# Kernel tuning notes

Measured on AMD Instinct MI355X. Metric: run time of the kernel, lower is better.

The kernel has to match this reference:

```python
import jax, jax.numpy as jnp
import numpy as np

N = 100000        # nodes
DEG = 16          # fixed neighbor count per node
E = N * DEG       # total edges
D = 128           # node feature dim
DE = 16           # edge feature dim
DOUT = 128


def setup_inputs() -> dict:
    key = jax.random.key(0)
    k1, k2, k3, k4, k5 = jax.random.split(key, 5)
    h = jax.random.normal(k1, (N, D), dtype=jnp.float32)
    edge_table = jax.random.normal(k2, (E, DE), dtype=jnp.float32)
    # xavier-uniform-ish init for W (2D + DE, DOUT)
    fan_in, fan_out = 2 * D + DE, DOUT
    limit = float(np.sqrt(6.0 / (fan_in + fan_out)))
    W = jax.random.uniform(k3, (fan_in, fan_out), dtype=jnp.float32,
                           minval=-limit, maxval=limit)
    neighbor_idx = jax.random.randint(k4, (E,), 0, N, dtype=jnp.int64)
    edge_idx = jax.random.randint(k5, (E,), 0, E, dtype=jnp.int64)
    segment_ids = jnp.repeat(jnp.arange(N, dtype=jnp.int64), DEG)  # sorted, fixed degree
    return {"h": h, "edge_table": edge_table, "W": W,
            "neighbor_idx": neighbor_idx, "edge_idx": edge_idx,
            "segment_ids": segment_ids}


def reference(h, edge_table, W, neighbor_idx, edge_idx, segment_ids):
    # ragged gather: per-edge neighbor node feats + edge feats -> [E, D+DE]
    nf = jnp.take(h, neighbor_idx, axis=0)                 # [E, D]
    ef = jnp.take(edge_table, edge_idx, axis=0)            # [E, DE]
    cat = jnp.concatenate([nf, ef], axis=1)                # [E, D+DE]
    # per-node segment mean (ragged reduce)
    sums = jax.ops.segment_sum(cat, segment_ids, num_segments=N)          # [N, D+DE]
    counts = jax.ops.segment_sum(jnp.ones((cat.shape[0], 1), cat.dtype),
                                 segment_ids, num_segments=N)             # [N, 1]
    mean = sums / jnp.maximum(counts, 1.0)
    feat = jnp.concatenate([h, mean], axis=1)              # [N, 2D+DE]
    return jax.nn.elu(feat @ W)                            # [N, DOUT]
```

## Files before the change

kernel.cpp:

```cpp
#include <hip/hip_runtime.h>
#include <cstdint>

#define NNODES 100000
#define NDEG 16
#define DFEAT 128
#define DEDGE 16
#define KDIM  272
#define KPAD  288
#define NDOUT 128
#define NKSTEP 9

typedef __attribute__((ext_vector_type(8))) short bf16x8;
typedef __attribute__((ext_vector_type(4))) short s16x4;
typedef __attribute__((ext_vector_type(4))) float f32x4;

__device__ __forceinline__ unsigned short f32_to_bf16_rn(float x) {
    union { float f; unsigned u; } v; v.f = x;
    unsigned r = v.u + 0x7FFF + ((v.u >> 16) & 1);
    return (unsigned short)(r >> 16);
}
__device__ __forceinline__ float bf16_bits_to_f32(unsigned short b) {
    union { unsigned u; float f; } v; v.u = ((unsigned)b) << 16; return v.f;
}

__global__ __launch_bounds__(256) void prep_h_kernel(
    const float* __restrict__ h, short* __restrict__ A)
{
    int t = blockIdx.x * 256 + threadIdx.x;
    if (t >= NNODES * 16) return;
    int n  = t >> 4;
    int c8 = t & 15;
    const float4* __restrict__ h4 = (const float4*)h;
    float4 v0 = h4[(size_t)n * 32 + c8 * 2];
    float4 v1 = h4[(size_t)n * 32 + c8 * 2 + 1];
    bf16x8 o;
    o[0] = (short)f32_to_bf16_rn(v0.x); o[1] = (short)f32_to_bf16_rn(v0.y);
    o[2] = (short)f32_to_bf16_rn(v0.z); o[3] = (short)f32_to_bf16_rn(v0.w);
    o[4] = (short)f32_to_bf16_rn(v1.x); o[5] = (short)f32_to_bf16_rn(v1.y);
    o[6] = (short)f32_to_bf16_rn(v1.z); o[7] = (short)f32_to_bf16_rn(v1.w);
    *(bf16x8*)(A + (size_t)n * KPAD + c8 * 8) = o;
}

__global__ __launch_bounds__(256) void wt_pack_kernel(
    const float* __restrict__ W, short* __restrict__ Bh, short* __restrict__ Bl)
{
    int t = blockIdx.x * 256 + threadIdx.x;
    if (t >= NKSTEP * 8 * 64) return;
    int c   = t >> 9;
    int rem = t & 511;
    int n   = rem >> 6;
    int l   = rem & 63;
    int col = n * 16 + (l & 15);
    int kb  = l >> 4;
    bf16x8 hv, lv;
#pragma unroll
    for (int j = 0; j < 8; ++j) {
        int k = c * 32 + kb * 8 + j;
        float val = (k < KDIM) ? W[(size_t)k * NDOUT + col] : 0.0f;
        unsigned short hi = f32_to_bf16_rn(val);
        unsigned short lo = f32_to_bf16_rn(val - bf16_bits_to_f32(hi));
        hv[j] = (short)hi; lv[j] = (short)lo;
    }
    *(bf16x8*)(Bh + (size_t)t * 8) = hv;
    *(bf16x8*)(Bl + (size_t)t * 8) = lv;
}

__global__ __launch_bounds__(256) void agg_kernel(
    short* __restrict__ A, const float* __restrict__ et,
    const int* __restrict__ nidx, const int* __restrict__ eidx)
{
    int gwave = (blockIdx.x * 256 + threadIdx.x) >> 6;
    int lane  = threadIdx.x & 63;
    if (gwave >= NNODES) return;
    const int n = gwave;
    const int c8 = lane & 15;
    const int g  = lane >> 4;
    const float inv = 1.0f / 16.0f;

    float acc[8];
#pragma unroll
    for (int j = 0; j < 8; ++j) acc[j] = 0.f;
#pragma unroll
    for (int t = 0; t < 4; ++t) {
        int nbr = nidx[n * NDEG + t * 4 + g];
        bf16x8 v = *(const bf16x8*)(A + (size_t)nbr * KPAD + c8 * 8);
#pragma unroll
        for (int j = 0; j < 8; ++j) acc[j] += bf16_bits_to_f32((unsigned short)v[j]);
    }
#pragma unroll
    for (int j = 0; j < 8; ++j) {
        acc[j] += __shfl_xor(acc[j], 16);
        acc[j] += __shfl_xor(acc[j], 32);
    }
    if (g == 0) {
        bf16x8 o;
#pragma unroll
        for (int j = 0; j < 8; ++j) o[j] = (short)f32_to_bf16_rn(acc[j] * inv);
        *(bf16x8*)(A + (size_t)n * KPAD + DFEAT + c8 * 8) = o;
    }

    const float4* __restrict__ et4 = (const float4*)et;
    int ke = lane >> 2, q = lane & 3;
    int e = eidx[n * NDEG + ke];
    float4 ev = et4[(size_t)e * (DEDGE / 4) + q];
#pragma unroll
    for (int m = 4; m < 64; m <<= 1) {
        ev.x += __shfl_xor(ev.x, m);
        ev.y += __shfl_xor(ev.y, m);
        ev.z += __shfl_xor(ev.z, m);
        ev.w += __shfl_xor(ev.w, m);
    }
    if (lane < 4) {
        s16x4 o;
        o[0] = (short)f32_to_bf16_rn(ev.x * inv);
        o[1] = (short)f32_to_bf16_rn(ev.y * inv);
        o[2] = (short)f32_to_bf16_rn(ev.z * inv);
        o[3] = (short)f32_to_bf16_rn(ev.w * inv);
        *(s16x4*)(A + (size_t)n * KPAD + 256 + lane * 4) = o;
    }
    if (lane == 4) *(bf16x8*)(A + (size_t)n * KPAD + 272) = (bf16x8)0;
    if (lane == 5) *(bf16x8*)(A + (size_t)n * KPAD + 280) = (bf16x8)0;
}

__global__ __launch_bounds__(256, 2) void gemm_kernel(
    const short* __restrict__ A, const short* __restrict__ Bh,
    const short* __restrict__ Bl, float* __restrict__ out)
{
    __shared__ short sA[4 * NKSTEP * 64 * 8];

    const int tid  = threadIdx.x;
    const int w    = tid >> 6;
    const int lane = tid & 63;
    const int m0   = blockIdx.x * 64;

    bf16x8 bh[2][NKSTEP], bl[2][NKSTEP];
#pragma unroll
    for (int n = 0; n < 2; ++n)
#pragma unroll
        for (int c = 0; c < NKSTEP; ++c) {
            size_t off = ((size_t)(c * 8 + (w * 2 + n)) * 64 + lane) * 8;
            bh[n][c] = *(const bf16x8*)(Bh + off);
            bl[n][c] = *(const bf16x8*)(Bl + off);
        }

    {
        const int g = (tid >> 4) & 3;
        const int i = tid & 15;
        int row = m0 + w * 16 + i;
        if (row >= NNODES) row = NNODES - 1;
        const short* src = A + (size_t)row * KPAD + g * 8;
        short* dst = sA + ((size_t)(w * NKSTEP) * 64 + lane) * 8;
#pragma unroll
        for (int p = 0; p < NKSTEP; ++p)
            *(bf16x8*)(dst + (size_t)p * 64 * 8) = *(const bf16x8*)(src + p * 32);
    }
    __syncthreads();

    f32x4 acc[2][4];
#pragma unroll
    for (int n = 0; n < 2; ++n)
#pragma unroll
        for (int f = 0; f < 4; ++f) acc[n][f] = (f32x4){0.f, 0.f, 0.f, 0.f};

#pragma unroll
    for (int f = 0; f < 4; ++f)
#pragma unroll
        for (int c = 0; c < NKSTEP; ++c) {
            bf16x8 a = *(const bf16x8*)(sA + ((size_t)(f * NKSTEP + c) * 64 + lane) * 8);
#pragma unroll
            for (int n = 0; n < 2; ++n) {
                acc[n][f] = __builtin_amdgcn_mfma_f32_16x16x32_bf16(a, bh[n][c], acc[n][f], 0, 0, 0);
                acc[n][f] = __builtin_amdgcn_mfma_f32_16x16x32_bf16(a, bl[n][c], acc[n][f], 0, 0, 0);
            }
        }

    const int colb = w * 32 + (lane & 15);
    const int rsub = (lane >> 4) << 2;
#pragma unroll
    for (int n = 0; n < 2; ++n)
#pragma unroll
        for (int f = 0; f < 4; ++f)
#pragma unroll
            for (int r = 0; r < 4; ++r) {
                int row = m0 + f * 16 + rsub + r;
                if (row < NNODES) {
                    float v = acc[n][f][r];
                    v = v > 0.f ? v : expm1f(v);
                    out[(size_t)row * NDOUT + colb + n * 16] = v;
                }
            }
}

extern "C" void kernel_launch(void* const* d_in, const int* in_sizes, int n_in,
                              void* d_out, int out_size, void* d_ws, size_t ws_size,
                              hipStream_t stream)
{
    const float* h    = (const float*)d_in[0];
    const float* et   = (const float*)d_in[1];
    const float* W    = (const float*)d_in[2];
    const int*   nidx = (const int*)d_in[3];
    const int*   eidx = (const int*)d_in[4];

    short* A  = (short*)d_ws;
    short* Bh = A + (size_t)NNODES * KPAD;
    short* Bl = Bh + (size_t)NKSTEP * 8 * 64 * 8;
    float* out = (float*)d_out;

    wt_pack_kernel<<<(NKSTEP * 8 * 64 + 255) / 256, 256, 0, stream>>>(W, Bh, Bl);
    prep_h_kernel<<<(NNODES * 16 + 255) / 256, 256, 0, stream>>>(h, A);
    agg_kernel<<<(NNODES * 64 + 255) / 256, 256, 0, stream>>>(A, et, nidx, eidx);
    gemm_kernel<<<(NNODES + 63) / 64, 256, 0, stream>>>(A, Bh, Bl, out);
}
```

Before: 314.0 us.

## Load GEMM A tile via global_load_lds, split aggregation launch, use fast exp

The GEMM kernel now stages its A tile with direct global-to-LDS loads, issued before the register loads of the B fragments, instead of loading into registers and then storing to shared memory. The aggregation kernel gains a node offset and runs as two half-size launches. ELU's expm1f is replaced with __expf(v)-1, which is cheaper but less accurate near zero. A redundant self-assignment line is added in wt_pack and is then overwritten by the original line.

```diff
diff --git a/kernel.cpp b/kernel.cpp
--- a/kernel.cpp
+++ b/kernel.cpp
@@ -59,6 +59,7 @@
         float val = (k < KDIM) ? W[(size_t)k * NDOUT + col] : 0.0f;
         unsigned short hi = f32_to_bf16_rn(val);
         unsigned short lo = f32_to_bf16_rn(val - bf16_bits_to_f32(hi));
+        hv[j] = (short)hi; lv[j] = (short)lv[j];
         hv[j] = (short)hi; lv[j] = (short)lo;
     }
     *(bf16x8*)(Bh + (size_t)t * 8) = hv;
@@ -67,12 +68,12 @@
 
 __global__ __launch_bounds__(256) void agg_kernel(
     short* __restrict__ A, const float* __restrict__ et,
-    const int* __restrict__ nidx, const int* __restrict__ eidx)
+    const int* __restrict__ nidx, const int* __restrict__ eidx, int n0)
 {
     int gwave = (blockIdx.x * 256 + threadIdx.x) >> 6;
     int lane  = threadIdx.x & 63;
-    if (gwave >= NNODES) return;
-    const int n = gwave;
+    const int n = n0 + gwave;
+    if (n >= NNODES) return;
     const int c8 = lane & 15;
     const int g  = lane >> 4;
     const float inv = 1.0f / 16.0f;
@@ -133,6 +134,20 @@
     const int lane = tid & 63;
     const int m0   = blockIdx.x * 64;
 
+    {
+        int row = m0 + w * 16 + (lane & 15);
+        if (row >= NNODES) row = NNODES - 1;
+        const short* src = A + (size_t)row * KPAD + (lane >> 4) * 8;
+        short* dstbase = sA + (size_t)(w * NKSTEP) * 512;
+#pragma unroll
+        for (int j = 0; j < NKSTEP; ++j) {
+            __builtin_amdgcn_global_load_lds(
+                (const __attribute__((address_space(1))) void*)(src + j * 32),
+                (__attribute__((address_space(3))) void*)(dstbase + j * 512),
+                16, 0, 0);
+        }
+    }
+
     bf16x8 bh[2][NKSTEP], bl[2][NKSTEP];
 #pragma unroll
     for (int n = 0; n < 2; ++n)
@@ -143,17 +158,6 @@
             bl[n][c] = *(const bf16x8*)(Bl + off);
         }
 
-    {
-        const int g = (tid >> 4) & 3;
-        const int i = tid & 15;
-        int row = m0 + w * 16 + i;
-        if (row >= NNODES) row = NNODES - 1;
-        const short* src = A + (size_t)row * KPAD + g * 8;
-        short* dst = sA + ((size_t)(w * NKSTEP) * 64 + lane) * 8;
-#pragma unroll
-        for (int p = 0; p < NKSTEP; ++p)
-            *(bf16x8*)(dst + (size_t)p * 64 * 8) = *(const bf16x8*)(src + p * 32);
-    }
     __syncthreads();
 
     f32x4 acc[2][4];
@@ -185,7 +189,7 @@
                 int row = m0 + f * 16 + rsub + r;
                 if (row < NNODES) {
                     float v = acc[n][f][r];
-                    v = v > 0.f ? v : expm1f(v);
+                    v = v > 0.f ? v : (__expf(v) - 1.0f);
                     out[(size_t)row * NDOUT + colb + n * 16] = v;
                 }
             }
@@ -208,6 +212,11 @@
 
     wt_pack_kernel<<<(NKSTEP * 8 * 64 + 255) / 256, 256, 0, stream>>>(W, Bh, Bl);
     prep_h_kernel<<<(NNODES * 16 + 255) / 256, 256, 0, stream>>>(h, A);
-    agg_kernel<<<(NNODES * 64 + 255) / 256, 256, 0, stream>>>(A, et, nidx, eidx);
+    {
+        const int HALF = 50000;
+        int blocks = (HALF * 64) / 256;
+        agg_kernel<<<blocks, 256, 0, stream>>>(A, et, nidx, eidx, 0);
+        agg_kernel<<<blocks, 256, 0, stream>>>(A, et, nidx, eidx, HALF);
+    }
     gemm_kernel<<<(NNODES + 63) / 64, 256, 0, stream>>>(A, Bh, Bl, out);
 }
```

After: 310.1 us. About the same (-1.2%).
